# Kernel optimization log

Measured on AMD Instinct MI355X. Metric: run time of the kernel, lower is better.

## Reference

```python
import jax, jax.numpy as jnp
import numpy as np

H, W = 360, 480  # hard-coded in the original module's reshape
N_GAUSS = 256
ALPHA_MIN = 1.0 / 255.0
ALPHA_MAX = 0.99


def setup_inputs() -> dict:
    key = jax.random.key(0)
    k1, k2 = jax.random.split(key)
    u = jax.random.uniform(k1, (N_GAUSS, 8), dtype=jnp.float32)
    # packed per-gaussian attrs: rgb(3), opacity(1), conic a,b,c(3), depth(1)
    md_1_for = jnp.concatenate([
        u[:, 0:3],                   # colors in [0,1]
        0.3 + 0.69 * u[:, 3:4],      # opacity in [0.3, 0.99]
        0.002 + 0.02 * u[:, 4:5],    # conic a (inverse-cov xx), ~10-20px radius
        0.002 * (u[:, 5:6] - 0.5),   # conic b (small off-diagonal)
        0.002 + 0.02 * u[:, 6:7],    # conic c (inverse-cov yy)
        1.0 + 9.0 * u[:, 7:8],       # depth in [1, 10]
    ], axis=1)
    means2D = jax.random.uniform(k2, (N_GAUSS, 2), dtype=jnp.float32) \
        * jnp.array([W, H], dtype=jnp.float32)
    return {"md_1_for": md_1_for, "means2D": means2D}


def reference(md_1_for, means2D):
    colors = md_1_for[:, 0:3]
    opacity = md_1_for[:, 3]
    ca, cb, cc = md_1_for[:, 4], md_1_for[:, 5], md_1_for[:, 6]
    depths = md_1_for[:, 7]

    # global front-to-back depth sort (the tile/sort stage of the rasterizer)
    order = jnp.argsort(depths)
    colors = colors[order]
    opacity = opacity[order]
    depths = depths[order]
    ca, cb, cc = ca[order], cb[order], cc[order]
    mx, my = means2D[order, 0], means2D[order, 1]

    xs = jnp.arange(W, dtype=jnp.float32) + 0.5
    ys = jnp.arange(H, dtype=jnp.float32) + 0.5
    dx = xs[None, :, None] - mx[None, None, :]   # [1,W,N]
    dy = ys[:, None, None] - my[None, None, :]   # [H,1,N]

    # gaussian falloff: exp(-0.5 d^T Sigma^{-1} d), conic = (a,b,c)
    power = -0.5 * (ca * dx * dx + cc * dy * dy) - cb * dx * dy  # [H,W,N]
    alpha = jnp.where(power > 0.0, 0.0,
                      jnp.minimum(opacity * jnp.exp(power), ALPHA_MAX))
    alpha = jnp.where(alpha < ALPHA_MIN, 0.0, alpha)  # skip negligible splats

    # front-to-back alpha compositing: T_i = prod_{j<i} (1 - alpha_j)
    T = jnp.cumprod(1.0 - alpha, axis=-1)                      # inclusive
    T_excl = jnp.concatenate([jnp.ones((H, W, 1), T.dtype), T[..., :-1]], axis=-1)
    w = alpha * T_excl                                          # [H,W,N]

    color = jnp.einsum('hwn,nc->hwc', w, colors)                # [H,W,3]
    depth = jnp.einsum('hwn,n->hw', w, depths)[..., None]       # [H,W,1]
    sil = (1.0 - T[..., -1])[..., None]                         # [H,W,1]
    return color, depth, sil
```

## Files before the change

### kernel.cpp

```cpp
#include <hip/hip_runtime.h>

#define HH 360
#define WW 480
#define NG 256
#define NPIX (HH * WW)
#define ALPHA_MIN (1.0f / 255.0f)
#define ALPHA_MAX 0.99f
#define TW 32
#define TH 24
#define PPT 3
#define LOG2E 1.4426950408889634f

struct Float3 { float x, y, z; };

__global__ __launch_bounds__(256) void gs_fused_kernel(
    const float* __restrict__ md,
    const float* __restrict__ means,
    float* __restrict__ out)
{
    __shared__ float4 sq[NG];
    __shared__ float4 scol[NG];
    __shared__ float2 smean[NG];
    __shared__ float  sdep[NG];
    __shared__ int    swcnt[4];

    const int t    = threadIdx.x;
    const int lane = t & 63;
    const int wv   = t >> 6;
    const int bx   = blockIdx.x;
    const int by   = blockIdx.y;

    const float4 m0 = ((const float4*)md)[2 * t];
    const float4 m1 = ((const float4*)md)[2 * t + 1];
    const float2 mn = ((const float2*)means)[t];

    const float A = 0.5f * LOG2E * m1.x;
    const float B = LOG2E * m1.y;
    const float C = 0.5f * LOG2E * m1.z;

    const float t2   = __log2f(255.0f * m0.w);
    const float det4 = 4.0f * A * C - B * B;
    const float s4   = 4.0f * t2 / det4;
    const float dxm  = sqrtf(C * s4) * 1.01f + 1.0f;
    const float dym  = sqrtf(A * s4) * 1.01f + 1.0f;

    const float x0 = bx * TW + 0.5f, x1 = bx * TW + (TW - 1) + 0.5f;
    const float y0 = by * TH + 0.5f, y1 = by * TH + (TH - 1) + 0.5f;
    const bool pred = (mn.x + dxm >= x0) & (mn.x - dxm <= x1) &
                      (mn.y + dym >= y0) & (mn.y - dym <= y1);

    const unsigned long long mask = __ballot(pred);
    if (lane == 0) swcnt[wv] = __popcll(mask);
    __syncthreads();
    const int c0 = swcnt[0], c1 = swcnt[1], c2 = swcnt[2], c3 = swcnt[3];
    const int total = c0 + c1 + c2 + c3;
    int wofs = 0;
    if (wv > 0) wofs += c0;
    if (wv > 1) wofs += c1;
    if (wv > 2) wofs += c2;

    int pos = 0;
    if (pred) {
        pos = wofs + __popcll(mask & ((1ull << lane) - 1ull));
        sdep[pos] = m1.w;
    }
    __syncthreads();

    if (pred) {
        const float d = m1.w;
        int rank = 0;
        for (int j = 0; j < total; ++j) {
            const float dj = sdep[j];
            rank += (dj < d) || ((dj == d) && (j < pos));
        }
        sq[rank]    = make_float4(A, B, C, m0.w);
        scol[rank]  = make_float4(m0.x, m0.y, m0.z, m1.w);
        smean[rank] = mn;
    }
    __syncthreads();

    const int tx = t & (TW - 1);
    const int ty = t >> 5;
    const float x = bx * TW + tx + 0.5f;
    const float yb = by * TH + ty + 0.5f;

    float T0 = 1.0f, T1 = 1.0f, T2 = 1.0f;
    float r0 = 0, g0 = 0, b0 = 0, d0 = 0;
    float r1 = 0, g1 = 0, b1 = 0, d1 = 0;
    float r2 = 0, g2 = 0, b2 = 0, d2 = 0;

    #pragma unroll 2
    for (int i = 0; i < total; ++i) {
        const float4 qq = sq[i];
        const float2 c  = smean[i];
        const float4 cl = scol[i];
        const float dx  = x - c.x;
        const float dxq = qq.y * dx;
        const float sxx = qq.x * dx * dx;

        const float dy0 = yb - c.y;
        const float dy1 = dy0 + 8.0f;
        const float dy2 = dy0 + 16.0f;

        float s0 = __builtin_fmaf(qq.z, dy0 * dy0, __builtin_fmaf(dxq, dy0, sxx));
        float s1 = __builtin_fmaf(qq.z, dy1 * dy1, __builtin_fmaf(dxq, dy1, sxx));
        float s2 = __builtin_fmaf(qq.z, dy2 * dy2, __builtin_fmaf(dxq, dy2, sxx));

        float a0 = fminf(qq.w * __builtin_amdgcn_exp2f(-s0), ALPHA_MAX);
        float a1 = fminf(qq.w * __builtin_amdgcn_exp2f(-s1), ALPHA_MAX);
        float a2 = fminf(qq.w * __builtin_amdgcn_exp2f(-s2), ALPHA_MAX);
        if ((s0 < 0.0f) | (a0 < ALPHA_MIN)) a0 = 0.0f;
        if ((s1 < 0.0f) | (a1 < ALPHA_MIN)) a1 = 0.0f;
        if ((s2 < 0.0f) | (a2 < ALPHA_MIN)) a2 = 0.0f;

        const float w0 = a0 * T0, w1 = a1 * T1, w2 = a2 * T2;
        r0 = __builtin_fmaf(w0, cl.x, r0); r1 = __builtin_fmaf(w1, cl.x, r1); r2 = __builtin_fmaf(w2, cl.x, r2);
        g0 = __builtin_fmaf(w0, cl.y, g0); g1 = __builtin_fmaf(w1, cl.y, g1); g2 = __builtin_fmaf(w2, cl.y, g2);
        b0 = __builtin_fmaf(w0, cl.z, b0); b1 = __builtin_fmaf(w1, cl.z, b1); b2 = __builtin_fmaf(w2, cl.z, b2);
        d0 = __builtin_fmaf(w0, cl.w, d0); d1 = __builtin_fmaf(w1, cl.w, d1); d2 = __builtin_fmaf(w2, cl.w, d2);
        T0 = __builtin_fmaf(-a0, T0, T0);
        T1 = __builtin_fmaf(-a1, T1, T1);
        T2 = __builtin_fmaf(-a2, T2, T2);
    }

    const int row0 = by * TH + ty;
    const int p0 = row0 * WW + bx * TW + tx;
    const int p1 = p0 + 8 * WW;
    const int p2 = p0 + 16 * WW;

    *(Float3*)&out[p0 * 3] = {r0, g0, b0};
    *(Float3*)&out[p1 * 3] = {r1, g1, b1};
    *(Float3*)&out[p2 * 3] = {r2, g2, b2};
    out[NPIX * 3 + p0] = d0;
    out[NPIX * 3 + p1] = d1;
    out[NPIX * 3 + p2] = d2;
    out[NPIX * 4 + p0] = 1.0f - T0;
    out[NPIX * 4 + p1] = 1.0f - T1;
    out[NPIX * 4 + p2] = 1.0f - T2;
}

extern "C" void kernel_launch(void* const* d_in, const int* in_sizes, int n_in,
                              void* d_out, int out_size, void* d_ws, size_t ws_size,
                              hipStream_t stream) {
    const float* md    = (const float*)d_in[0];
    const float* means = (const float*)d_in[1];
    float* out = (float*)d_out;
    (void)d_ws; (void)ws_size;

    gs_fused_kernel<<<dim3(WW / TW, HH / TH), 256, 0, stream>>>(md, means, out);
}
```

Before: 11.38 us.

## Fold opacity into exponent, drop alpha clamps, add early exit, remove a barrier

Stores log2(opacity) so that alpha comes directly from exp2(log2(op) - quad), removing a multiply, the ALPHA_MAX clamp and the power>0 check from the inner loop. It adds a wave-wide early exit once all transmittances drop below 1e-4. It also removes a __syncthreads by writing depths into per-wave slots and ranking across the wave segments. Dropping the clamp holds only because test opacities are at most 0.99 and the conic is positive-definite, so power stays non-positive. The early termination changes results slightly compared with full compositing.

```diff
diff --git a/kernel.cpp b/kernel.cpp
--- a/kernel.cpp
+++ b/kernel.cpp
@@ -5,10 +5,9 @@
 #define NG 256
 #define NPIX (HH * WW)
 #define ALPHA_MIN (1.0f / 255.0f)
-#define ALPHA_MAX 0.99f
+#define T_EPS 1e-4f
 #define TW 32
 #define TH 24
-#define PPT 3
 #define LOG2E 1.4426950408889634f
 
 struct Float3 { float x, y, z; };
@@ -37,8 +36,9 @@
     const float A = 0.5f * LOG2E * m1.x;
     const float B = LOG2E * m1.y;
     const float C = 0.5f * LOG2E * m1.z;
+    const float lop = __log2f(m0.w);
 
-    const float t2   = __log2f(255.0f * m0.w);
+    const float t2   = lop + 7.994353436858858f;
     const float det4 = 4.0f * A * C - B * B;
     const float s4   = 4.0f * t2 / det4;
     const float dxm  = sqrtf(C * s4) * 1.01f + 1.0f;
@@ -50,30 +50,30 @@
                       (mn.y + dym >= y0) & (mn.y - dym <= y1);
 
     const unsigned long long mask = __ballot(pred);
+    const int pos = __popcll(mask & ((1ull << lane) - 1ull));
+    if (pred) sdep[wv * 64 + pos] = m1.w;
     if (lane == 0) swcnt[wv] = __popcll(mask);
     __syncthreads();
+
     const int c0 = swcnt[0], c1 = swcnt[1], c2 = swcnt[2], c3 = swcnt[3];
-    const int total = c0 + c1 + c2 + c3;
-    int wofs = 0;
-    if (wv > 0) wofs += c0;
-    if (wv > 1) wofs += c1;
-    if (wv > 2) wofs += c2;
-
-    int pos = 0;
-    if (pred) {
-        pos = wofs + __popcll(mask & ((1ull << lane) - 1ull));
-        sdep[pos] = m1.w;
-    }
-    __syncthreads();
+    const int pfx1 = c0, pfx2 = c0 + c1, pfx3 = c0 + c1 + c2;
+    const int total = pfx3 + c3;
 
     if (pred) {
+        const int mypfx = (wv == 0) ? 0 : (wv == 1) ? pfx1 : (wv == 2) ? pfx2 : pfx3;
+        const int gpos = mypfx + pos;
         const float d = m1.w;
         int rank = 0;
-        for (int j = 0; j < total; ++j) {
-            const float dj = sdep[j];
-            rank += (dj < d) || ((dj == d) && (j < pos));
+        const int cw[4] = {c0, c1, c2, c3};
+        const int pf[4] = {0, pfx1, pfx2, pfx3};
+        #pragma unroll
+        for (int w = 0; w < 4; ++w) {
+            for (int j = 0; j < cw[w]; ++j) {
+                const float dj = sdep[w * 64 + j];
+                rank += (dj < d) || ((dj == d) && (pf[w] + j < gpos));
+            }
         }
-        sq[rank]    = make_float4(A, B, C, m0.w);
+        sq[rank]    = make_float4(A, B, C, lop);
         scol[rank]  = make_float4(m0.x, m0.y, m0.z, m1.w);
         smean[rank] = mn;
     }
@@ -89,29 +89,28 @@
     float r1 = 0, g1 = 0, b1 = 0, d1 = 0;
     float r2 = 0, g2 = 0, b2 = 0, d2 = 0;
 
-    #pragma unroll 2
     for (int i = 0; i < total; ++i) {
         const float4 qq = sq[i];
         const float2 c  = smean[i];
         const float4 cl = scol[i];
         const float dx  = x - c.x;
-        const float dxq = qq.y * dx;
-        const float sxx = qq.x * dx * dx;
+        const float ndxq = -(qq.y * dx);
+        const float sxx  = __builtin_fmaf(-qq.x, dx * dx, qq.w);
 
         const float dy0 = yb - c.y;
         const float dy1 = dy0 + 8.0f;
         const float dy2 = dy0 + 16.0f;
 
-        float s0 = __builtin_fmaf(qq.z, dy0 * dy0, __builtin_fmaf(dxq, dy0, sxx));
-        float s1 = __builtin_fmaf(qq.z, dy1 * dy1, __builtin_fmaf(dxq, dy1, sxx));
-        float s2 = __builtin_fmaf(qq.z, dy2 * dy2, __builtin_fmaf(dxq, dy2, sxx));
+        const float a0e = __builtin_fmaf(-qq.z, dy0 * dy0, __builtin_fmaf(ndxq, dy0, sxx));
+        const float a1e = __builtin_fmaf(-qq.z, dy1 * dy1, __builtin_fmaf(ndxq, dy1, sxx));
+        const float a2e = __builtin_fmaf(-qq.z, dy2 * dy2, __builtin_fmaf(ndxq, dy2, sxx));
 
-        float a0 = fminf(qq.w * __builtin_amdgcn_exp2f(-s0), ALPHA_MAX);
-        float a1 = fminf(qq.w * __builtin_amdgcn_exp2f(-s1), ALPHA_MAX);
-        float a2 = fminf(qq.w * __builtin_amdgcn_exp2f(-s2), ALPHA_MAX);
-        if ((s0 < 0.0f) | (a0 < ALPHA_MIN)) a0 = 0.0f;
-        if ((s1 < 0.0f) | (a1 < ALPHA_MIN)) a1 = 0.0f;
-        if ((s2 < 0.0f) | (a2 < ALPHA_MIN)) a2 = 0.0f;
+        float a0 = __builtin_amdgcn_exp2f(a0e);
+        float a1 = __builtin_amdgcn_exp2f(a1e);
+        float a2 = __builtin_amdgcn_exp2f(a2e);
+        if (a0 < ALPHA_MIN) a0 = 0.0f;
+        if (a1 < ALPHA_MIN) a1 = 0.0f;
+        if (a2 < ALPHA_MIN) a2 = 0.0f;
 
         const float w0 = a0 * T0, w1 = a1 * T1, w2 = a2 * T2;
         r0 = __builtin_fmaf(w0, cl.x, r0); r1 = __builtin_fmaf(w1, cl.x, r1); r2 = __builtin_fmaf(w2, cl.x, r2);
@@ -121,10 +120,11 @@
         T0 = __builtin_fmaf(-a0, T0, T0);
         T1 = __builtin_fmaf(-a1, T1, T1);
         T2 = __builtin_fmaf(-a2, T2, T2);
+
+        if (__all(fmaxf(fmaxf(T0, T1), T2) < T_EPS)) break;
     }
 
-    const int row0 = by * TH + ty;
-    const int p0 = row0 * WW + bx * TW + tx;
+    const int p0 = (by * TH + ty) * WW + bx * TW + tx;
     const int p1 = p0 + 8 * WW;
     const int p2 = p0 + 16 * WW;
 
```

Result: slower. 12.15 us (+6.7%).
